# Optimization experiments

Measured on AMD Instinct MI355X. Metric: run time of the kernel, lower is better.

Reference implementation:

```python
import jax, jax.numpy as jnp
import numpy as np

B, C, HH, WW = 256, 1024, 7, 7
S = HH * WW            # 49 tokens
D = 1024               # hidden_size
L = 2                  # encoder_layers (nhead arg, swapped in source)
H = 2                  # attention heads (num_layers arg, swapped in source)
HD = D // H            # 512 head dim
FF = 1024              # encoder_ffn_dim
OUT = 1024             # head output
EPS = 1e-5


def setup_inputs() -> dict:
    key = jax.random.key(0)
    ks = jax.random.split(key, 10)
    n = lambda k, shape: jax.random.normal(k, shape, jnp.float32) * 0.02
    return dict(
        x=jax.random.normal(ks[0], (B, C, HH, WW), jnp.float32),
        pos_emb=n(ks[1], (S, D)),
        ln1_s=jnp.ones((L, D), jnp.float32), ln1_b=jnp.zeros((L, D), jnp.float32),
        wq=n(ks[2], (L, D, D)), wk=n(ks[3], (L, D, D)),
        wv=n(ks[4], (L, D, D)), wo=n(ks[5], (L, D, D)),
        ln2_s=jnp.ones((L, D), jnp.float32), ln2_b=jnp.zeros((L, D), jnp.float32),
        w1=n(ks[6], (L, D, FF)), b1=jnp.zeros((L, FF), jnp.float32),
        w2=n(ks[7], (L, FF, D)), b2=jnp.zeros((L, D), jnp.float32),
        lnf_s=jnp.ones((D,), jnp.float32), lnf_b=jnp.zeros((D,), jnp.float32),
        head_w=n(ks[8], (S * D, OUT)), head_b=jnp.zeros((OUT,), jnp.float32),
    )


def _ln(x, s, b):
    m = jnp.mean(x, axis=-1, keepdims=True)
    v = jnp.var(x, axis=-1, keepdims=True)
    return (x - m) * jax.lax.rsqrt(v + EPS) * s + b


def reference(x, pos_emb, ln1_s, ln1_b, wq, wk, wv, wo, ln2_s, ln2_b,
              w1, b1, w2, b2, lnf_s, lnf_b, head_w, head_b):
    b = x.shape[0]
    # flatten HxW then permute -> [B, S, D] token sequence
    h = x.reshape(b, C, S).transpose(0, 2, 1)
    # BigBirdPegasus encoder: learned pos emb added to inputs_embeds (no scaling path)
    h = h + pos_emb[None, :, :]
    scale = 1.0 / jnp.sqrt(jnp.float32(HD))
    for i in range(L):
        # --- self-attention block (pre-LN); seq_len=49 triggers original_full attention ---
        r = h
        hn = _ln(h, ln1_s[i], ln1_b[i])
        q = (hn @ wq[i]).reshape(b, S, H, HD)
        k = (hn @ wk[i]).reshape(b, S, H, HD)
        v = (hn @ wv[i]).reshape(b, S, H, HD)
        scores = jnp.einsum('bqhd,bkhd->bhqk', q, k) * scale
        attn = jax.nn.softmax(scores, axis=-1)
        ctx = jnp.einsum('bhqk,bkhd->bqhd', attn, v).reshape(b, S, D)
        h = r + ctx @ wo[i]
        # --- feed-forward block (pre-LN, gelu_new) ---
        r = h
        hn = _ln(h, ln2_s[i], ln2_b[i])
        hn = jax.nn.gelu(hn @ w1[i] + b1[i], approximate=True)
        h = r + hn @ w2[i] + b2[i]
    # BigBirdPegasus applies layernorm_embedding AFTER the layer stack
    h = _ln(h, lnf_s, lnf_b)
    # flatten + linear + relu head
    out = jax.nn.relu(h.reshape(b, S * D) @ head_w + head_b)
    return out
```

## Files before the change

kernel.cpp:

```cpp
#include <hip/hip_runtime.h>
#include <hip/hip_bf16.h>
#include <stdint.h>

#define Bq 256
#define Sq 49
#define Dq 1024
#define Hq 2
#define HDq 512
#define Mq (Bq*Sq)
#define KHEADq (Sq*Dq)
#define STq 3072

typedef unsigned short u16;
typedef short bf16x8 __attribute__((ext_vector_type(8)));
typedef float f32x4 __attribute__((ext_vector_type(4)));

__device__ inline u16 f2bf(float f){
  union { float f; uint32_t u; } c; c.f = f;
  uint32_t r = c.u + 0x7FFFu + ((c.u >> 16) & 1u);
  return (u16)(r >> 16);
}
__device__ inline float bf2f(u16 h){
  union { uint32_t u; float f; } c; c.u = ((uint32_t)h) << 16;
  return c.f;
}

#define GLOAD_LDS16(gp, lp) \
  __builtin_amdgcn_global_load_lds((__attribute__((address_space(1))) void*)(gp), \
                                   (__attribute__((address_space(3))) void*)(lp), 16, 0, 0)
#define MFMA16(a,b,c) __builtin_amdgcn_mfma_f32_16x16x32_bf16(a,b,c,0,0,0)

__global__ __launch_bounds__(256) void prep_kernel(const float* __restrict__ x,
    const float* __restrict__ pos, u16* __restrict__ h, float2* __restrict__ pstat,
    u16* __restrict__ qkv){
  __shared__ float t[49*129];
  int b = blockIdx.x, c0 = blockIdx.y*128;
  int tid = threadIdx.x, lane = tid & 63, wave = tid >> 6;
  if(b == 0){
    uint4* pz = (uint4*)(qkv + (size_t)Mq*STq + (size_t)blockIdx.y*6144);
    pz[tid] = make_uint4(0,0,0,0);
    pz[256+tid] = make_uint4(0,0,0,0);
    pz[512+tid] = make_uint4(0,0,0,0);
  }
  const float* xb = x + (size_t)b*(Dq*Sq) + (size_t)c0*Sq;
  #pragma unroll
  for(int i=0;i<32;i++){
    int cc = wave + i*4;
    if(lane < Sq) t[lane*129 + cc] = xb[(size_t)cc*Sq + lane];
  }
  __syncthreads();
  #pragma unroll
  for(int p=0;p<25;p++){
    int idx = p*256 + tid;
    int s = idx >> 7, cc = idx & 127;
    if(s < Sq){
      float hv = t[s*129 + cc] + pos[s*Dq + c0 + cc];
      h[((size_t)b*Sq + s)*Dq + c0 + cc] = f2bf(hv);
      t[s*129 + cc] = hv;
    }
  }
  __syncthreads();
  int r = tid >> 2, qd = tid & 3;
  if(r < Sq){
    float S=0.f, Q=0.f;
    for(int cc=qd; cc<128; cc+=4){ float vv = t[r*129+cc]; S+=vv; Q+=vv*vv; }
    S += __shfl_xor(S,1); Q += __shfl_xor(Q,1);
    S += __shfl_xor(S,2); Q += __shfl_xor(Q,2);
    if(qd==0){ float2 pp; pp.x=S; pp.y=Q; pstat[(size_t)blockIdx.y*Mq + b*Sq + r] = pp; }
  }
}

__global__ __launch_bounds__(256) void ln_kernel(const u16* __restrict__ hin,
    const float* __restrict__ sc, const float* __restrict__ bi, u16* __restrict__ outp){
  int wave = threadIdx.x >> 6, lane = threadIdx.x & 63;
  int row = blockIdx.x*4 + wave;
  const u16* p = hin + (size_t)row*Dq + lane*16;
  uint4 t0 = *(const uint4*)p;
  uint4 t1 = *(const uint4*)(p + 8);
  float v[16];
  {
    uint32_t wds[8] = {t0.x,t0.y,t0.z,t0.w,t1.x,t1.y,t1.z,t1.w};
    #pragma unroll
    for(int i=0;i<8;i++){
      v[2*i]   = bf2f((u16)(wds[i] & 0xffff));
      v[2*i+1] = bf2f((u16)(wds[i] >> 16));
    }
  }
  float s=0.f, sq=0.f;
  #pragma unroll
  for(int i=0;i<16;i++){ s += v[i]; sq += v[i]*v[i]; }
  #pragma unroll
  for(int o=32;o>=1;o>>=1){ s += __shfl_xor(s,o); sq += __shfl_xor(sq,o); }
  float mean = s * (1.f/Dq);
  float var  = sq * (1.f/Dq) - mean*mean;
  float rs = rsqrtf(var + 1e-5f);
  int c0 = lane*16;
  uint32_t w[8];
  #pragma unroll
  for(int i=0;i<8;i++){
    u16 lo = f2bf((v[2*i]   - mean)*rs*sc[c0+2*i]   + bi[c0+2*i]);
    u16 hi = f2bf((v[2*i+1] - mean)*rs*sc[c0+2*i+1] + bi[c0+2*i+1]);
    w[i] = (uint32_t)lo | ((uint32_t)hi << 16);
  }
  uint4* ob = (uint4*)(outp + (size_t)row*Dq + c0);
  ob[0] = make_uint4(w[0],w[1],w[2],w[3]);
  ob[1] = make_uint4(w[4],w[5],w[6],w[7]);
}

__global__ void transp_all(const float* __restrict__ wq, const float* __restrict__ wk,
    const float* __restrict__ wv, const float* __restrict__ wo,
    const float* __restrict__ w1, const float* __restrict__ w2,
    const float* __restrict__ ln1s, const float* __restrict__ ln2s, u16* __restrict__ outp){
  __shared__ float t[32][33];
  int slot = blockIdx.z; int l = slot / 6, j = slot - l*6;
  const float* srcs[6] = {wq,wk,wv,wo,w1,w2};
  const float* in = srcs[j] + (size_t)l*Dq*Dq;
  const float* sc = (j<3) ? (ln1s + l*Dq) : (j==4 ? (ln2s + l*Dq) : nullptr);
  u16* o = outp + (size_t)slot*Dq*Dq;
  int k0 = blockIdx.x*32, n0 = blockIdx.y*32;
  int tx = threadIdx.x, ty = threadIdx.y;
  #pragma unroll
  for(int i=0;i<4;i++) t[ty+8*i][tx] = in[(size_t)(k0+ty+8*i)*Dq + n0+tx];
  __syncthreads();
  float sck = sc ? sc[k0+tx] : 1.f;
  #pragma unroll
  for(int i=0;i<4;i++) o[(size_t)(n0+ty+8*i)*Dq + k0+tx] = f2bf(t[tx][ty+8*i] * sck);
}

__global__ __launch_bounds__(256) void uv_all_kernel(const float* __restrict__ wq,
    const float* __restrict__ wk, const float* __restrict__ wv, const float* __restrict__ w1,
    const float* __restrict__ ln1s, const float* __restrict__ ln1b,
    const float* __restrict__ ln2s, const float* __restrict__ ln2b, float* __restrict__ uvbuf){
  __shared__ float2 red[8][32];
  int t = threadIdx.x;
  int colg = blockIdx.x*32 + (t & 31);
  int ks = t >> 5;
  int l = colg >> 12, col = colg & 4095;
  int j = col >> 10, n = col & 1023;
  const float* srcs[4] = {wq, wk, wv, w1};
  const float* src = srcs[j] + (size_t)l*Dq*Dq;
  const float* sc = (j<3 ? ln1s : ln2s) + l*Dq;
  const float* bi = (j<3 ? ln1b : ln2b) + l*Dq;
  float u=0.f, v=0.f;
  for(int k=ks*128;k<ks*128+128;k++){
    float val = src[(size_t)k*Dq + n];
    u += sc[k]*val; v += bi[k]*val;
  }
  float2 pp; pp.x=u; pp.y=v;
  red[ks][t&31] = pp;
  __syncthreads();
  if(t < 32){
    float U=0.f, V=0.f;
    #pragma unroll
    for(int s2=0;s2<8;s2++){ float2 q2 = red[s2][t]; U+=q2.x; V+=q2.y; }
    uvbuf[(size_t)(blockIdx.x*32 + t)*2]   = U;
    uvbuf[(size_t)(blockIdx.x*32 + t)*2+1] = V;
  }
}

template<int EPI>
__global__ __launch_bounds__(512, 2) void gemm_nt2(
    const u16* __restrict__ A, int lda,
    const u16* __restrict__ Bt, int ldb,
    void* __restrict__ Cout, const u16* __restrict__ resid,
    const float* __restrict__ bias, int ldc,
    const float2* __restrict__ pstat_in, int nchunk,
    const float* __restrict__ uvp, float2* __restrict__ pstat_out,
    int total, int gxT)
{
  __shared__ u16 lds[65536];
  int tid = threadIdx.x, lane = tid & 63;
  int wave = tid >> 6;
  int wm = wave >> 2, wn = wave & 3;
  int l15 = lane & 15, l4 = lane >> 4;
  int swz = (l15 & 7) << 4;

  int srow = tid >> 3, scolb = (tid & 7) * 16;
  int scolx = scolb ^ ((srow & 7) << 4);

  for(int w = blockIdx.x; w < total; w += gridDim.x){
    int qq = total >> 3, rr = total & 7;
    int xcd = w & 7, idx = w >> 3;
    int wgid = (xcd < rr ? xcd*(qq+1) : rr*(qq+1) + (xcd-rr)*qq) + idx;
    int bx = wgid % gxT, by = wgid / gxT;
    int m0 = by*256, n0 = bx*256;

    auto stage2 = [&](int d, int kt, int h){
      #pragma unroll
      for(int cc=0; cc<2; cc++){
        int c = 2*h + cc;
        if(c < 4){
          int row = c*64 + srow;
          const u16* src = A + (size_t)(m0+row)*lda + kt*64 + (scolx>>1);
          GLOAD_LDS16(src, &lds[d*16384 + c*4096 + tid*8]);
        } else {
          int c4 = c - 4;
          int row = c4*64 + srow;
          const u16* src = Bt + (size_t)(n0+row)*ldb + kt*64 + (scolx>>1);
          GLOAD_LDS16(src, &lds[32768 + d*16384 + c4*4096 + tid*8]);
        }
      }
    };
    auto rdA = [&](int d, int i, int s)->bf16x8{
      int row = wm*128 + i*16 + l15;
      int byt = row*128 + ((s*64 + l4*16) ^ swz);
      return *(const bf16x8*)((const char*)lds + d*32768 + byt);
    };
    auto rdB = [&](int d, int n, int s)->bf16x8{
      int row = wn*64 + n*16 + l15;
      int byt = row*128 + ((s*64 + l4*16) ^ swz);
      return *(const bf16x8*)((const char*)lds + 65536 + d*32768 + byt);
    };

    f32x4 acc[8][4] = {};

    __syncthreads();
    #pragma unroll
    for(int h=0;h<4;h++) stage2(0, 0, h);

    for(int t=0; t<16; ++t){
      int d = t & 1;
      bf16x8 bfr[4][2];
      if(t < 15){
        stage2(d^1, t+1, 0);
        asm volatile("s_waitcnt vmcnt(2)" ::: "memory");
      } else {
        asm volatile("s_waitcnt vmcnt(0)" ::: "memory");
      }
      __builtin_amdgcn_sched_barrier(0);
      __builtin_amdgcn_s_barrier();
      bfr[0][0]=rdB(d,0,0); bfr[0][1]=rdB(d,0,1);
      bfr[1][0]=rdB(d,1,0); bfr[1][1]=rdB(d,1,1);
      bf16x8 a0s0=rdA(d,0,0), a0s1=rdA(d,0,1), a1s0=rdA(d,1,0), a1s1=rdA(d,1,1);
      __builtin_amdgcn_s_setprio(1);
      acc[0][0]=MFMA16(a0s0,bfr[0][0],acc[0][0]); acc[0][0]=MFMA16(a0s1,bfr[0][1],acc[0][0]);
      acc[0][1]=MFMA16(a0s0,bfr[1][0],acc[0][1]); acc[0][1]=MFMA16(a0s1,bfr[1][1],acc[0][1]);
      acc[1][0]=MFMA16(a1s0,bfr[0][0],acc[1][0]); acc[1][0]=MFMA16(a1s1,bfr[0][1],acc[1][0]);
      acc[1][1]=MFMA16(a1s0,bfr[1][0],acc[1][1]); acc[1][1]=MFMA16(a1s1,bfr[1][1],acc[1][1]);
      __builtin_amdgcn_s_setprio(0);
      __builtin_amdgcn_s_barrier();
      bfr[2][0]=rdB(d,2,0); bfr[2][1]=rdB(d,2,1);
      bfr[3][0]=rdB(d,3,0); bfr[3][1]=rdB(d,3,1);
      if(t < 15) stage2(d^1, t+1, 1);
      __builtin_amdgcn_s_barrier();
      __builtin_amdgcn_s_setprio(1);
      acc[0][2]=MFMA16(a0s0,bfr[2][0],acc[0][2]); acc[0][2]=MFMA16(a0s1,bfr[2][1],acc[0][2]);
      acc[0][3]=MFMA16(a0s0,bfr[3][0],acc[0][3]); acc[0][3]=MFMA16(a0s1,bfr[3][1],acc[0][3]);
      acc[1][2]=MFMA16(a1s0,bfr[2][0],acc[1][2]); acc[1][2]=MFMA16(a1s1,bfr[2][1],acc[1][2]);
      acc[1][3]=MFMA16(a1s0,bfr[3][0],acc[1][3]); acc[1][3]=MFMA16(a1s1,bfr[3][1],acc[1][3]);
      __builtin_amdgcn_s_setprio(0);
      __builtin_amdgcn_s_barrier();
      #pragma unroll
      for(int q=1;q<4;q++){
        bf16x8 c0s0=rdA(d,2*q,0), c0s1=rdA(d,2*q,1), c1s0=rdA(d,2*q+1,0), c1s1=rdA(d,2*q+1,1);
        if(t < 15 && q < 3) stage2(d^1, t+1, q+1);
        __builtin_amdgcn_s_barrier();
        __builtin_amdgcn_s_setprio(1);
        #pragma unroll
        for(int n=0;n<4;n++){
          acc[2*q][n]   = MFMA16(c0s0, bfr[n][0], acc[2*q][n]);
          acc[2*q][n]   = MFMA16(c0s1, bfr[n][1], acc[2*q][n]);
          acc[2*q+1][n] = MFMA16(c1s0, bfr[n][0], acc[2*q+1][n]);
          acc[2*q+1][n] = MFMA16(c1s1, bfr[n][1], acc[2*q+1][n]);
        }
        __builtin_amdgcn_s_setprio(0);
        __builtin_amdgcn_s_barrier();
      }
    }

    if constexpr (EPI == 1){
      float2* statsS = (float2*)((char*)lds + 49152);
      float* slotf = (float*)((char*)lds + wave*4096);
      float bv[4];
      #pragma unroll
      for(int n=0;n<4;n++) bv[n] = bias ? bias[n0 + wn*64 + n*16 + l15] : 0.f;
      #pragma unroll
      for(int i=0;i<8;i++){
        #pragma unroll
        for(int n=0;n<4;n++)
          #pragma unroll
          for(int r=0;r<4;r++)
            slotf[(l4*4+r)*64 + n*16 + l15] = acc[i][n][r] + bv[n];
        #pragma unroll
        for(int st=0;st<2;st++){
          int u = st*64 + lane;
          int row = u >> 3, c8 = (u & 7)*8;
          f32x4 lo = *(const f32x4*)&slotf[row*64 + c8];
          f32x4 hi = *(const f32x4*)&slotf[row*64 + c8 + 4];
          size_t o = (size_t)(m0 + wm*128 + i*16 + row)*ldc + n0 + wn*64 + c8;
          bf16x8 rb = *(const bf16x8*)(resid + o);
          bf16x8 ov; float fs=0.f, fq=0.f;
          #pragma unroll
          for(int j=0;j<4;j++){
            float a_ = lo[j] + bf2f((u16)rb[j]);
            float b_ = hi[j] + bf2f((u16)rb[4+j]);
            ov[j]   = (short)f2bf(a_);
            ov[4+j] = (short)f2bf(b_);
            fs += a_ + b_; fq += a_*a_ + b_*b_;
          }
          *(bf16x8*)((u16*)Cout + o) = ov;
          fs += __shfl_xor(fs,1); fq += __shfl_xor(fq,1);
          fs += __shfl_xor(fs,2); fq += __shfl_xor(fq,2);
          fs += __shfl_xor(fs,4); fq += __shfl_xor(fq,4);
          if((lane&7)==0){
            float2 pp; pp.x=fs; pp.y=fq;
            statsS[(wm*128 + i*16 + st*8 + (lane>>3))*4 + wn] = pp;
          }
        }
      }
      __syncthreads();
      if(tid < 256){
        float S=0.f, Q=0.f;
        #pragma unroll
        for(int w2_=0;w2_<4;w2_++){ float2 pp = statsS[tid*4+w2_]; S+=pp.x; Q+=pp.y; }
        float2 pp; pp.x=S; pp.y=Q;
        pstat_out[(size_t)bx*Mq + m0 + tid] = pp;
      }
    } else {
      float2* lstat = (float2*)((char*)lds + 49152);
      if(tid < 256){
        float S=0.f, Q=0.f;
        for(int c=0;c<nchunk;c++){ float2 pp = pstat_in[(size_t)c*Mq + m0 + tid]; S+=pp.x; Q+=pp.y; }
        float mean = S*(1.f/1024.f);
        float var  = Q*(1.f/1024.f) - mean*mean;
        float2 sm; sm.x = rsqrtf(var + 1e-5f); sm.y = mean;
        lstat[tid] = sm;
      }
      __syncthreads();
      u16* slot = (u16*)((char*)lds + wave*2048);
      float uvv[4][2], bv[4];
      #pragma unroll
      for(int n=0;n<4;n++){
        int ncol = n0 + wn*64 + n*16 + l15;
        float2 uv2 = ((const float2*)uvp)[ncol];
        uvv[n][0] = uv2.x; uvv[n][1] = uv2.y;
        if constexpr (EPI == 2) bv[n] = bias[ncol];
      }
      #pragma unroll
      for(int i=0;i<8;i++){
        #pragma unroll
        for(int n=0;n<4;n++)
          #pragma unroll
          for(int r=0;r<4;r++){
            float2 sm = lstat[wm*128 + i*16 + l4*4 + r];
            float va = sm.x*acc[i][n][r] - sm.x*sm.y*uvv[n][0] + uvv[n][1];
            u16 ov;
            if constexpr (EPI == 0){
              ov = f2bf(va);
            } else {
              float xg = va + bv[n];
              float tg = tanhf(0.79788456080286536f*(xg + 0.044715f*xg*xg*xg));
              ov = f2bf(0.5f*xg*(1.f+tg));
            }
            slot[(l4*4+r)*64 + n*16 + l15] = ov;
          }
        #pragma unroll
        for(int st=0;st<2;st++){
          int u = st*64 + lane;
          int row = u >> 3, c8 = (u & 7)*8;
          bf16x8 v8 = *(const bf16x8*)&slot[row*64 + c8];
          *(bf16x8*)((u16*)Cout + (size_t)(m0 + wm*128 + i*16 + row)*ldc + n0 + wn*64 + c8) = v8;
        }
      }
    }
  }
}

__global__ __launch_bounds__(256, 3) void gemm_head(
    const u16* __restrict__ A, const float* __restrict__ W,
    u16* __restrict__ parts)
{
  __shared__ u16 sA[2][128*32];
  int tid = threadIdx.x, lane = tid & 63;
  int wave = tid >> 6;
  int wm = wave >> 1, wn = wave & 1;
  int l15 = lane & 15, l4 = lane >> 4;
  int bx = blockIdx.x, by = blockIdx.y, z = blockIdx.z;
  int n0 = bx*128, m0 = by*128;
  size_t abase = (size_t)m0*KHEADq + (size_t)z*1024;
  f32x4 acc[4][4] = {};
  const float* wp = W + ((size_t)z*1024 + (size_t)l4*8)*1024 + n0 + wn*64 + l15;

  auto stageA = [&](int d, int kt){
    #pragma unroll
    for(int c=0;c<2;c++){
      int s2 = c*256+tid;
      GLOAD_LDS16(A + abase + (size_t)(s2>>2)*KHEADq + kt*32 + (s2&3)*8, &sA[d][s2*8]);
    }
  };
  float wA[4][8], wB[4][8];
  auto loadW = [&](float (&dst)[4][8], int kt){
    #pragma unroll
    for(int f=0;f<4;f++)
      #pragma unroll
      for(int jj=0;jj<8;jj++)
        dst[f][jj] = wp[(size_t)(kt*32+jj)*1024 + f*16];
  };
  auto compute = [&](int d, float (&wreg)[4][8]){
    bf16x8 bfr[4];
    #pragma unroll
    for(int f=0;f<4;f++){
      bf16x8 bv;
      #pragma unroll
      for(int jj=0;jj<8;jj++)
        bv[jj] = __builtin_bit_cast(short, __float2bfloat16(wreg[f][jj]));
      bfr[f] = bv;
    }
    bf16x8 af[4];
    #pragma unroll
    for(int i=0;i<4;i++)
      af[i] = *(const bf16x8*)&sA[d][(wm*64 + i*16 + l15)*32 + l4*8];
    #pragma unroll
    for(int i=0;i<4;i++)
      #pragma unroll
      for(int j=0;j<4;j++)
        acc[i][j] = MFMA16(af[i], bfr[j], acc[i][j]);
  };

  stageA(0, 0);
  loadW(wA, 0);
  for(int k2=0; k2<16; ++k2){
    int kt = 2*k2;
    stageA(1, kt+1);
    loadW(wB, kt+1);
    asm volatile("s_waitcnt vmcnt(34)" ::: "memory");
    __builtin_amdgcn_s_barrier();
    compute(0, wA);
    __builtin_amdgcn_s_barrier();
    if(k2 < 15){
      stageA(0, kt+2);
      loadW(wA, kt+2);
      asm volatile("s_waitcnt vmcnt(34)" ::: "memory");
    } else {
      asm volatile("s_waitcnt vmcnt(0)" ::: "memory");
    }
    __builtin_amdgcn_s_barrier();
    compute(1, wB);
    __builtin_amdgcn_s_barrier();
  }

  u16* slot = &sA[0][wave*1024];
  u16* base = parts + (size_t)z*(Bq*1024);
  #pragma unroll
  for(int i=0;i<4;i++){
    #pragma unroll
    for(int j=0;j<4;j++)
      #pragma unroll
      for(int rr=0;rr<4;rr++)
        slot[(l4*4+rr)*64 + j*16 + l15] = f2bf(acc[i][j][rr]);
    #pragma unroll
    for(int st=0;st<2;st++){
      int u = st*64 + lane;
      int row = u >> 3, c8 = (u & 7)*8;
      bf16x8 v8 = *(const bf16x8*)&slot[row*64 + c8];
      *(bf16x8*)(base + (size_t)(m0 + wm*64 + i*16 + row)*1024 + n0 + wn*64 + c8) = v8;
    }
  }
}

__global__ __launch_bounds__(256) void attn_kernel(u16* __restrict__ qkv)
{
  __shared__ float sS[64][65];
  __shared__ u16 sP[64][64];
  int bh = blockIdx.x;
  int b = bh >> 1, h = bh & 1;
  int tid = threadIdx.x, lane = tid & 63, wave = tid >> 6;
  int l15 = lane & 15, l4 = lane >> 4;
  f32x4 zero4 = {0.f,0.f,0.f,0.f};
  bf16x8 zb = {0,0,0,0,0,0,0,0};
  f32x4 acc[4];
  #pragma unroll
  for(int i=0;i<4;i++) acc[i] = zero4;
  int srow = wave*16 + l15;
  const u16* qp = qkv + (size_t)(b*Sq + srow)*STq + h*HDq + l4*8;
  const u16* kbase = qkv + (size_t)b*Sq*STq + Dq + h*HDq + l4*8;
  for(int kt=0;kt<16;kt++){
    bf16x8 aq = (srow < Sq) ? *(const bf16x8*)(qp + kt*32) : zb;
    #pragma unroll
    for(int fn=0;fn<4;fn++){
      int s2 = fn*16 + l15;
      bf16x8 bk = (s2 < Sq) ? *(const bf16x8*)(kbase + (size_t)s2*STq + kt*32) : zb;
      acc[fn] = MFMA16(aq, bk, acc[fn]);
    }
  }
  const float scale = 0.04419417382415922f;
  #pragma unroll
  for(int fn=0;fn<4;fn++)
    #pragma unroll
    for(int r=0;r<4;r++)
      sS[wave*16 + l4*4 + r][fn*16 + l15] = acc[fn][r]*scale;
  __syncthreads();
  {
    int r = tid >> 2, qd = tid & 3;
    float mx = -1e30f;
    for(int j=qd;j<Sq;j+=4) mx = fmaxf(mx, sS[r][j]);
    mx = fmaxf(mx, __shfl_xor(mx,1));
    mx = fmaxf(mx, __shfl_xor(mx,2));
    float sum = 0.f;
    for(int j=qd;j<Sq;j+=4){ float e = __expf(sS[r][j]-mx); sS[r][j]=e; sum+=e; }
    sum += __shfl_xor(sum,1);
    sum += __shfl_xor(sum,2);
    float inv = 1.f/sum;
    for(int j=qd;j<64;j+=4) sP[r][j] = (j<Sq)? f2bf(sS[r][j]*inv) : (u16)0;
  }
  __syncthreads();
  bf16x8 ap[2];
  #pragma unroll
  for(int kt2=0;kt2<2;kt2++)
    ap[kt2] = *(const bf16x8*)&sP[wave*16 + l15][kt2*32 + l4*8];
  const u16* vbp = qkv + (size_t)b*Sq*STq + 2*Dq + h*HDq + l15;
  u16* cb = qkv + (size_t)b*Sq*STq + h*HDq;
  for(int fn=0;fn<32;fn++){
    f32x4 c4 = zero4;
    #pragma unroll
    for(int kt2=0;kt2<2;kt2++){
      const u16* vp = vbp + fn*16 + (size_t)(kt2*32 + l4*8)*STq;
      bf16x8 bv;
      #pragma unroll
      for(int jj=0;jj<8;jj++) bv[jj] = (short)vp[(size_t)jj*STq];
      c4 = MFMA16(ap[kt2], bv, c4);
    }
    #pragma unroll
    for(int r=0;r<4;r++){
      int s = wave*16 + l4*4 + r;
      if(s < Sq) cb[(size_t)s*STq + fn*16 + l15] = f2bf(c4[r]);
    }
  }
}

__global__ __launch_bounds__(256) void head_finalize(const u16* __restrict__ parts,
    const float* __restrict__ hb, float* __restrict__ outp){
  int idx = blockIdx.x*256 + threadIdx.x;
  float s = hb[idx & 1023];
  #pragma unroll
  for(int z=0;z<49;z++) s += bf2f(parts[(size_t)z*(Bq*1024) + idx]);
  outp[idx] = fmaxf(s, 0.f);
}

extern "C" void kernel_launch(void* const* d_in, const int* in_sizes, int n_in,
                              void* d_out, int out_size, void* d_ws, size_t ws_size,
                              hipStream_t stream) {
  (void)in_sizes; (void)n_in; (void)out_size;
  const float* x    = (const float*)d_in[0];
  const float* pos  = (const float*)d_in[1];
  const float* ln1s = (const float*)d_in[2];
  const float* ln1b = (const float*)d_in[3];
  const float* wq   = (const float*)d_in[4];
  const float* wk   = (const float*)d_in[5];
  const float* wv   = (const float*)d_in[6];
  const float* wo   = (const float*)d_in[7];
  const float* ln2s = (const float*)d_in[8];
  const float* ln2b = (const float*)d_in[9];
  const float* w1   = (const float*)d_in[10];
  const float* b1   = (const float*)d_in[11];
  const float* w2   = (const float*)d_in[12];
  const float* b2   = (const float*)d_in[13];
  const float* lnfs = (const float*)d_in[14];
  const float* lnfb = (const float*)d_in[15];
  const float* hw   = (const float*)d_in[16];
  const float* hb   = (const float*)d_in[17];
  float* out = (float*)d_out;

  char* ws = (char*)d_ws;
  size_t off = 0;
  auto carve = [&](size_t n) -> char* { char* p = ws + off; off += (n + 255) & ~(size_t)255; return p; };
  u16*   h     = (u16*)  carve((size_t)Mq*Dq*2);
  u16*   act0  = (u16*)  carve((size_t)Mq*Dq*2);
  u16*   act1  = (u16*)  carve((size_t)Mq*Dq*2);
  u16*   qkv   = (u16*)  carve((size_t)(Mq+16)*STq*2);
  u16*   wT    = (u16*)  carve((size_t)12*Dq*Dq*2);
  float2* pstat= (float2*)carve((size_t)8*Mq*sizeof(float2));
  float* uvbuf = (float*)carve((size_t)2*4096*2*4);
  u16*   parts = qkv;
  if (off > ws_size) return;

  prep_kernel<<<dim3(Bq, 8), 256, 0, stream>>>(x, pos, h, pstat, qkv);
  transp_all<<<dim3(32,32,12), dim3(32,8), 0, stream>>>(wq, wk, wv, wo, w1, w2, ln1s, ln2s, wT);
  uv_all_kernel<<<256, 256, 0, stream>>>(wq, wk, wv, w1, ln1s, ln1b, ln2s, ln2b, uvbuf);

  for(int l=0;l<2;l++){
    u16* qkvT = wT + (size_t)(l*6+0)*Dq*Dq;
    u16* woT  = wT + (size_t)(l*6+3)*Dq*Dq;
    u16* w1T  = wT + (size_t)(l*6+4)*Dq*Dq;
    u16* w2T  = wT + (size_t)(l*6+5)*Dq*Dq;
    const float* uvq = uvbuf + (size_t)l*8192;
    const float* uv1 = uvbuf + (size_t)l*8192 + 3072*2;

    gemm_nt2<0><<<512, 512, 0, stream>>>(h, Dq, qkvT, Dq, qkv, nullptr, nullptr, STq,
                                         pstat, (l==0)?8:4, uvq, nullptr, 588, 12);
    attn_kernel<<<Bq*Hq, 256, 0, stream>>>(qkv);
    gemm_nt2<1><<<196, 512, 0, stream>>>(qkv, STq, woT, Dq, h, h, nullptr, Dq,
                                         nullptr, 0, nullptr, pstat, 196, 4);
    gemm_nt2<2><<<196, 512, 0, stream>>>(h, Dq, w1T, Dq, act1, nullptr, b1 + l*Dq, Dq,
                                         pstat, 4, uv1, nullptr, 196, 4);
    gemm_nt2<1><<<196, 512, 0, stream>>>(act1, Dq, w2T, Dq, h, h, b2 + l*Dq, Dq,
                                         nullptr, 0, nullptr, pstat, 196, 4);
  }

  ln_kernel<<<Mq/4, 256, 0, stream>>>(h, lnfs, lnfb, act0);
  gemm_head<<<dim3(8,2,49), 256, 0, stream>>>(act0, hw, parts);
  head_finalize<<<1024, 256, 0, stream>>>(parts, hb, out);
}
```

Baseline: 681.5 us.

## Merge setup kernels into one launch and stage V through LDS in attention

Folds the prep, weight-transpose and uv-reduction kernels into a single launch that dispatches on block index, removing two launches and the gaps between them. The attention kernel now stages V in shared memory in two 256-column halves, using coalesced 8-byte loads, instead of doing strided 2-byte global gathers for every MFMA operand. The second half is prefetched into registers while softmax runs. This raises LDS and register use in the attention kernel, which may lower occupancy.

```diff
diff --git a/kernel.cpp b/kernel.cpp
--- a/kernel.cpp
+++ b/kernel.cpp
@@ -30,43 +30,99 @@
                                    (__attribute__((address_space(3))) void*)(lp), 16, 0, 0)
 #define MFMA16(a,b,c) __builtin_amdgcn_mfma_f32_16x16x32_bf16(a,b,c,0,0,0)
 
-__global__ __launch_bounds__(256) void prep_kernel(const float* __restrict__ x,
-    const float* __restrict__ pos, u16* __restrict__ h, float2* __restrict__ pstat,
-    u16* __restrict__ qkv){
-  __shared__ float t[49*129];
-  int b = blockIdx.x, c0 = blockIdx.y*128;
-  int tid = threadIdx.x, lane = tid & 63, wave = tid >> 6;
-  if(b == 0){
-    uint4* pz = (uint4*)(qkv + (size_t)Mq*STq + (size_t)blockIdx.y*6144);
-    pz[tid] = make_uint4(0,0,0,0);
-    pz[256+tid] = make_uint4(0,0,0,0);
-    pz[512+tid] = make_uint4(0,0,0,0);
-  }
-  const float* xb = x + (size_t)b*(Dq*Sq) + (size_t)c0*Sq;
-  #pragma unroll
-  for(int i=0;i<32;i++){
-    int cc = wave + i*4;
-    if(lane < Sq) t[lane*129 + cc] = xb[(size_t)cc*Sq + lane];
-  }
-  __syncthreads();
-  #pragma unroll
-  for(int p=0;p<25;p++){
-    int idx = p*256 + tid;
-    int s = idx >> 7, cc = idx & 127;
-    if(s < Sq){
-      float hv = t[s*129 + cc] + pos[s*Dq + c0 + cc];
-      h[((size_t)b*Sq + s)*Dq + c0 + cc] = f2bf(hv);
-      t[s*129 + cc] = hv;
-    }
-  }
-  __syncthreads();
-  int r = tid >> 2, qd = tid & 3;
-  if(r < Sq){
-    float S=0.f, Q=0.f;
-    for(int cc=qd; cc<128; cc+=4){ float vv = t[r*129+cc]; S+=vv; Q+=vv*vv; }
-    S += __shfl_xor(S,1); Q += __shfl_xor(Q,1);
-    S += __shfl_xor(S,2); Q += __shfl_xor(Q,2);
-    if(qd==0){ float2 pp; pp.x=S; pp.y=Q; pstat[(size_t)blockIdx.y*Mq + b*Sq + r] = pp; }
+__global__ __launch_bounds__(256) void setup_kernel(
+    const float* __restrict__ x, const float* __restrict__ pos,
+    u16* __restrict__ h, float2* __restrict__ pstat, u16* __restrict__ qkv,
+    const float* __restrict__ wq, const float* __restrict__ wk,
+    const float* __restrict__ wv, const float* __restrict__ wo,
+    const float* __restrict__ w1, const float* __restrict__ w2,
+    const float* __restrict__ ln1s, const float* __restrict__ ln1b,
+    const float* __restrict__ ln2s, const float* __restrict__ ln2b,
+    u16* __restrict__ wT, float* __restrict__ uvbuf)
+{
+  __shared__ __align__(16) float smem[6336];
+  int bid = blockIdx.x;
+  int tid = threadIdx.x;
+  if(bid < 2048){
+    float* t = smem;
+    int b = bid >> 3, yy = bid & 7, c0 = yy*128;
+    int lane = tid & 63, wave = tid >> 6;
+    if(b == 0){
+      uint4* pz = (uint4*)(qkv + (size_t)Mq*STq + (size_t)yy*6144);
+      pz[tid] = make_uint4(0,0,0,0);
+      pz[256+tid] = make_uint4(0,0,0,0);
+      pz[512+tid] = make_uint4(0,0,0,0);
+    }
+    const float* xb = x + (size_t)b*(Dq*Sq) + (size_t)c0*Sq;
+    #pragma unroll
+    for(int i=0;i<32;i++){
+      int cc = wave + i*4;
+      if(lane < Sq) t[lane*129 + cc] = xb[(size_t)cc*Sq + lane];
+    }
+    __syncthreads();
+    #pragma unroll
+    for(int p=0;p<25;p++){
+      int idx = p*256 + tid;
+      int s = idx >> 7, cc = idx & 127;
+      if(s < Sq){
+        float hv = t[s*129 + cc] + pos[s*Dq + c0 + cc];
+        h[((size_t)b*Sq + s)*Dq + c0 + cc] = f2bf(hv);
+        t[s*129 + cc] = hv;
+      }
+    }
+    __syncthreads();
+    int r = tid >> 2, qd = tid & 3;
+    if(r < Sq){
+      float S=0.f, Q=0.f;
+      for(int cc=qd; cc<128; cc+=4){ float vv = t[r*129+cc]; S+=vv; Q+=vv*vv; }
+      S += __shfl_xor(S,1); Q += __shfl_xor(Q,1);
+      S += __shfl_xor(S,2); Q += __shfl_xor(Q,2);
+      if(qd==0){ float2 pp; pp.x=S; pp.y=Q; pstat[(size_t)yy*Mq + b*Sq + r] = pp; }
+    }
+  } else if(bid < 14336){
+    int j = bid - 2048;
+    int slot = j >> 10, jb = j & 1023;
+    int k0 = (jb & 31)*32, n0 = (jb >> 5)*32;
+    int l = slot / 6, jj = slot - l*6;
+    const float* srcs[6] = {wq,wk,wv,wo,w1,w2};
+    const float* in = srcs[jj] + (size_t)l*Dq*Dq;
+    const float* sc = (jj<3) ? (ln1s + l*Dq) : (jj==4 ? (ln2s + l*Dq) : nullptr);
+    u16* o = wT + (size_t)slot*Dq*Dq;
+    float (*t)[33] = (float(*)[33])smem;
+    int tx = tid & 31, ty = tid >> 5;
+    #pragma unroll
+    for(int i=0;i<4;i++) t[ty+8*i][tx] = in[(size_t)(k0+ty+8*i)*Dq + n0+tx];
+    __syncthreads();
+    float sck = sc ? sc[k0+tx] : 1.f;
+    #pragma unroll
+    for(int i=0;i<4;i++) o[(size_t)(n0+ty+8*i)*Dq + k0+tx] = f2bf(t[tx][ty+8*i] * sck);
+  } else {
+    int j = bid - 14336;
+    float2 (*red)[32] = (float2(*)[32])smem;
+    int t = tid;
+    int colg = j*32 + (t & 31);
+    int ks = t >> 5;
+    int l = colg >> 12, col = colg & 4095;
+    int jj = col >> 10, n = col & 1023;
+    const float* srcs[4] = {wq, wk, wv, w1};
+    const float* src = srcs[jj] + (size_t)l*Dq*Dq;
+    const float* sc = (jj<3 ? ln1s : ln2s) + l*Dq;
+    const float* bi = (jj<3 ? ln1b : ln2b) + l*Dq;
+    float u=0.f, v=0.f;
+    for(int k=ks*128;k<ks*128+128;k++){
+      float val = src[(size_t)k*Dq + n];
+      u += sc[k]*val; v += bi[k]*val;
+    }
+    float2 pp; pp.x=u; pp.y=v;
+    red[ks][t&31] = pp;
+    __syncthreads();
+    if(t < 32){
+      float U=0.f, V=0.f;
+      #pragma unroll
+      for(int s2=0;s2<8;s2++){ float2 q2 = red[s2][t]; U+=q2.x; V+=q2.y; }
+      uvbuf[(size_t)(j*32 + t)*2]   = U;
+      uvbuf[(size_t)(j*32 + t)*2+1] = V;
+    }
   }
 }
 
@@ -105,57 +161,6 @@
   uint4* ob = (uint4*)(outp + (size_t)row*Dq + c0);
   ob[0] = make_uint4(w[0],w[1],w[2],w[3]);
   ob[1] = make_uint4(w[4],w[5],w[6],w[7]);
-}
-
-__global__ void transp_all(const float* __restrict__ wq, const float* __restrict__ wk,
-    const float* __restrict__ wv, const float* __restrict__ wo,
-    const float* __restrict__ w1, const float* __restrict__ w2,
-    const float* __restrict__ ln1s, const float* __restrict__ ln2s, u16* __restrict__ outp){
-  __shared__ float t[32][33];
-  int slot = blockIdx.z; int l = slot / 6, j = slot - l*6;
-  const float* srcs[6] = {wq,wk,wv,wo,w1,w2};
-  const float* in = srcs[j] + (size_t)l*Dq*Dq;
-  const float* sc = (j<3) ? (ln1s + l*Dq) : (j==4 ? (ln2s + l*Dq) : nullptr);
-  u16* o = outp + (size_t)slot*Dq*Dq;
-  int k0 = blockIdx.x*32, n0 = blockIdx.y*32;
-  int tx = threadIdx.x, ty = threadIdx.y;
-  #pragma unroll
-  for(int i=0;i<4;i++) t[ty+8*i][tx] = in[(size_t)(k0+ty+8*i)*Dq + n0+tx];
-  __syncthreads();
-  float sck = sc ? sc[k0+tx] : 1.f;
-  #pragma unroll
-  for(int i=0;i<4;i++) o[(size_t)(n0+ty+8*i)*Dq + k0+tx] = f2bf(t[tx][ty+8*i] * sck);
-}
-
-__global__ __launch_bounds__(256) void uv_all_kernel(const float* __restrict__ wq,
-    const float* __restrict__ wk, const float* __restrict__ wv, const float* __restrict__ w1,
-    const float* __restrict__ ln1s, const float* __restrict__ ln1b,
-    const float* __restrict__ ln2s, const float* __restrict__ ln2b, float* __restrict__ uvbuf){
-  __shared__ float2 red[8][32];
-  int t = threadIdx.x;
-  int colg = blockIdx.x*32 + (t & 31);
-  int ks = t >> 5;
-  int l = colg >> 12, col = colg & 4095;
-  int j = col >> 10, n = col & 1023;
-  const float* srcs[4] = {wq, wk, wv, w1};
-  const float* src = srcs[j] + (size_t)l*Dq*Dq;
-  const float* sc = (j<3 ? ln1s : ln2s) + l*Dq;
-  const float* bi = (j<3 ? ln1b : ln2b) + l*Dq;
-  float u=0.f, v=0.f;
-  for(int k=ks*128;k<ks*128+128;k++){
-    float val = src[(size_t)k*Dq + n];
-    u += sc[k]*val; v += bi[k]*val;
-  }
-  float2 pp; pp.x=u; pp.y=v;
-  red[ks][t&31] = pp;
-  __syncthreads();
-  if(t < 32){
-    float U=0.f, V=0.f;
-    #pragma unroll
-    for(int s2=0;s2<8;s2++){ float2 q2 = red[s2][t]; U+=q2.x; V+=q2.y; }
-    uvbuf[(size_t)(blockIdx.x*32 + t)*2]   = U;
-    uvbuf[(size_t)(blockIdx.x*32 + t)*2+1] = V;
-  }
 }
 
 template<int EPI>
@@ -462,6 +467,7 @@
 {
   __shared__ float sS[64][65];
   __shared__ u16 sP[64][64];
+  __shared__ __align__(16) u16 sV[64*260 + 4];
   int bh = blockIdx.x;
   int b = bh >> 1, h = bh & 1;
   int tid = threadIdx.x, lane = tid & 63, wave = tid >> 6;
@@ -489,6 +495,14 @@
     #pragma unroll
     for(int r=0;r<4;r++)
       sS[wave*16 + l4*4 + r][fn*16 + l15] = acc[fn][r]*scale;
+  const u16* vsrc = qkv + (size_t)b*Sq*STq + 2*Dq + h*HDq;
+  #pragma unroll
+  for(int p=0;p<16;p++){
+    int i = p*256 + tid;
+    int row = i >> 6, ch = i & 63;
+    uint2 v2 = (row < Sq) ? *(const uint2*)(vsrc + (size_t)row*STq + ch*4) : make_uint2(0u,0u);
+    *(uint2*)&sV[row*260 + ch*4] = v2;
+  }
   __syncthreads();
   {
     int r = tid >> 2, qd = tid & 3;
@@ -503,21 +517,51 @@
     float inv = 1.f/sum;
     for(int j=qd;j<64;j+=4) sP[r][j] = (j<Sq)? f2bf(sS[r][j]*inv) : (u16)0;
   }
+  uint2 vreg[16];
+  #pragma unroll
+  for(int p=0;p<16;p++){
+    int i = p*256 + tid;
+    int row = i >> 6, ch = i & 63;
+    vreg[p] = (row < Sq) ? *(const uint2*)(vsrc + 256 + (size_t)row*STq + ch*4) : make_uint2(0u,0u);
+  }
   __syncthreads();
   bf16x8 ap[2];
   #pragma unroll
   for(int kt2=0;kt2<2;kt2++)
     ap[kt2] = *(const bf16x8*)&sP[wave*16 + l15][kt2*32 + l4*8];
-  const u16* vbp = qkv + (size_t)b*Sq*STq + 2*Dq + h*HDq + l15;
   u16* cb = qkv + (size_t)b*Sq*STq + h*HDq;
-  for(int fn=0;fn<32;fn++){
+  for(int fn=0;fn<16;fn++){
     f32x4 c4 = zero4;
     #pragma unroll
     for(int kt2=0;kt2<2;kt2++){
-      const u16* vp = vbp + fn*16 + (size_t)(kt2*32 + l4*8)*STq;
+      int rbase = kt2*32 + l4*8;
       bf16x8 bv;
       #pragma unroll
-      for(int jj=0;jj<8;jj++) bv[jj] = (short)vp[(size_t)jj*STq];
+      for(int jj=0;jj<8;jj++) bv[jj] = (short)sV[(rbase+jj)*260 + fn*16 + l15];
+      c4 = MFMA16(ap[kt2], bv, c4);
+    }
+    #pragma unroll
+    for(int r=0;r<4;r++){
+      int s = wave*16 + l4*4 + r;
+      if(s < Sq) cb[(size_t)s*STq + fn*16 + l15] = f2bf(c4[r]);
+    }
+  }
+  __syncthreads();
+  #pragma unroll
+  for(int p=0;p<16;p++){
+    int i = p*256 + tid;
+    int row = i >> 6, ch = i & 63;
+    *(uint2*)&sV[row*260 + ch*4] = vreg[p];
+  }
+  __syncthreads();
+  for(int fn=16;fn<32;fn++){
+    f32x4 c4 = zero4;
+    #pragma unroll
+    for(int kt2=0;kt2<2;kt2++){
+      int rbase = kt2*32 + l4*8;
+      bf16x8 bv;
+      #pragma unroll
+      for(int jj=0;jj<8;jj++) bv[jj] = (short)sV[(rbase+jj)*260 + (fn-16)*16 + l15];
       c4 = MFMA16(ap[kt2], bv, c4);
     }
     #pragma unroll
@@ -574,9 +618,8 @@
   u16*   parts = qkv;
   if (off > ws_size) return;
 
-  prep_kernel<<<dim3(Bq, 8), 256, 0, stream>>>(x, pos, h, pstat, qkv);
-  transp_all<<<dim3(32,32,12), dim3(32,8), 0, stream>>>(wq, wk, wv, wo, w1, w2, ln1s, ln2s, wT);
-  uv_all_kernel<<<256, 256, 0, stream>>>(wq, wk, wv, w1, ln1s, ln1b, ln2s, ln2b, uvbuf);
+  setup_kernel<<<14592, 256, 0, stream>>>(x, pos, h, pstat, qkv,
+      wq, wk, wv, wo, w1, w2, ln1s, ln1b, ln2s, ln2b, wT, uvbuf);
 
   for(int l=0;l<2;l++){
     u16* qkvT = wT + (size_t)(l*6+0)*Dq*Dq;
```

After: 670.7 us, median of 3. About the same (-1.6%).
